# Optimization experiments

Measured on AMD Instinct MI355X. Metric: run time of the kernel, lower is better.

## Reference

```python
import jax, jax.numpy as jnp
import numpy as np

B, NQ, NKV = 2, 2048, 2048
QUERY_DIM = 1024
CONTEXT_DIM = 1024
HEADS = 16
DIM_HEAD = 64
INNER = HEADS * DIM_HEAD
SCALE = DIM_HEAD ** -0.5


def setup_inputs() -> dict:
    key = jax.random.key(0)
    ks = jax.random.split(key, 9)
    x = jax.random.normal(ks[0], (B, NQ, QUERY_DIM), dtype=jnp.float32)
    context = jax.random.normal(ks[1], (B, NKV, CONTEXT_DIM), dtype=jnp.float32)
    tgt_mask = jax.random.randint(ks[2], (B, 1, NQ, NKV), 0, 2, dtype=jnp.int32)
    src_mask = jax.random.randint(ks[3], (B, 1, NKV), 0, 2) > 0  # bool [b,1,j]
    w = 0.02
    Wq = jax.random.normal(ks[4], (INNER, QUERY_DIM), dtype=jnp.float32) * w
    Wk = jax.random.normal(ks[5], (INNER, CONTEXT_DIM), dtype=jnp.float32) * w
    Wv = jax.random.normal(ks[6], (INNER, CONTEXT_DIM), dtype=jnp.float32) * w
    Wo = jax.random.normal(ks[7], (QUERY_DIM, INNER), dtype=jnp.float32) * w
    bo = jax.random.normal(ks[8], (QUERY_DIM,), dtype=jnp.float32) * w
    return {"x": x, "context": context, "tgt_mask": tgt_mask, "src_mask": src_mask,
            "Wq": Wq, "Wk": Wk, "Wv": Wv, "Wo": Wo, "bo": bo}


def reference(x, context, tgt_mask, src_mask, Wq, Wk, Wv, Wo, bo):
    b, nq, _ = x.shape
    nkv = context.shape[1]
    # Linear projections (torch Linear: y = x @ W.T), split into heads: b n (h d) -> b h n d
    q = jnp.einsum('bnc,ec->bne', x, Wq).reshape(b, nq, HEADS, DIM_HEAD).transpose(0, 2, 1, 3)
    k = jnp.einsum('bmc,ec->bme', context, Wk).reshape(b, nkv, HEADS, DIM_HEAD).transpose(0, 2, 1, 3)
    v = jnp.einsum('bmc,ec->bme', context, Wv).reshape(b, nkv, HEADS, DIM_HEAD).transpose(0, 2, 1, 3)
    sim = jnp.einsum('bhid,bhjd->bhij', q, k) * SCALE
    neg = -jnp.finfo(sim.dtype).max
    sim = jnp.where(tgt_mask == 0, neg, sim)                 # tgt_mask [b,1,i,j]
    sim = jnp.where(src_mask[:, None, :], sim, neg)          # src_mask [b,1,j] -> [b,1,1,j]
    attn = jax.nn.softmax(sim, axis=-1)
    out = jnp.einsum('bhij,bhjd->bhid', attn, v)
    out = out.transpose(0, 2, 1, 3).reshape(b, nq, INNER)    # b h n d -> b n (h d)
    return jnp.einsum('bne,oe->bno', out, Wo) + bo           # dropout=0 at inference
```

## Files before the change

kernel.cpp:

```cpp
#include <hip/hip_runtime.h>

typedef short short8 __attribute__((ext_vector_type(8)));
typedef float f32x4 __attribute__((ext_vector_type(4)));
typedef float f32x16 __attribute__((ext_vector_type(16)));
typedef unsigned u32x4 __attribute__((ext_vector_type(4)));

#define GLOAD_LDS(src, dst) \
  __builtin_amdgcn_global_load_lds((const __attribute__((address_space(1))) void*)(src), \
                                   (__attribute__((address_space(3))) void*)(dst), 16, 0, 0)

__device__ __forceinline__ unsigned short f2b(float f){
  __bf16 h = (__bf16)f;
  return __builtin_bit_cast(unsigned short, h);
}
__device__ __forceinline__ unsigned pk2(float a, float b){
  unsigned r;
  asm("v_cvt_pk_bf16_f32 %0, %1, %2" : "=v"(r) : "v"(a), "v"(b));
  return r;
}
__device__ __forceinline__ float fexp2(float x){
  return __builtin_amdgcn_exp2f(x);
}
__device__ __forceinline__ float b2f(unsigned short u){
  union { unsigned u; float f; } cv;
  cv.u = ((unsigned)u) << 16;
  return cv.f;
}

__global__ void detect_mask_dtype(const int* __restrict__ src, int* __restrict__ flag){
  const int t = threadIdx.x;
  unsigned f = 0;
  #pragma unroll
  for (int i = 0; i < 16; i++)
    f |= (((const unsigned*)src)[t * 16 + i] > 1u) ? 1u : 0u;
  const unsigned long long any = __ballot(f != 0u);
  if (t == 0) *flag = any ? 1 : 0;
}

__global__ __launch_bounds__(256) void prep(const float* __restrict__ x, const float* __restrict__ ctx,
    const float* __restrict__ wq, const float* __restrict__ wk, const float* __restrict__ wv,
    const float* __restrict__ wo, const int* __restrict__ tgt, const void* __restrict__ srcm,
    const int* __restrict__ flag,
    unsigned short* __restrict__ xb, unsigned short* __restrict__ cb, unsigned short* __restrict__ wqb,
    unsigned short* __restrict__ wkvb, unsigned short* __restrict__ wob,
    unsigned long long* __restrict__ mp){
  const int blk = blockIdx.x;
  if (blk < 12288){
    const int i = blk * 256 + threadIdx.x;
    const float* src; unsigned short* dst; int so, doff;
    if (i < 1048576)      { src = x;   dst = xb;   so = i;           doff = so; }
    else if (i < 2097152) { src = ctx; dst = cb;   so = i - 1048576; doff = so; }
    else if (i < 2359296) { src = wq;  dst = wqb;  so = i - 2097152; doff = so; }
    else if (i < 2621440) { src = wk;  dst = wkvb; so = i - 2359296; doff = so; }
    else if (i < 2883584) { src = wv;  dst = wkvb; so = i - 2621440; doff = so + 262144; }
    else                  { src = wo;  dst = wob;  so = i - 2883584; doff = so; }
    const float4 v = reinterpret_cast<const float4*>(src)[so];
    ushort4 o;
    o.x = f2b(v.x); o.y = f2b(v.y); o.z = f2b(v.z); o.w = f2b(v.w);
    reinterpret_cast<ushort4*>(dst)[doff] = o;
  } else {
    size_t gt = (size_t)(blk - 12288) * 256 + threadIdx.x;
    int j = (int)(gt & 2047);
    size_t bi = gt >> 11;
    int b = (int)(bi >> 11);
    bool s;
    if (*flag) s = ((const unsigned char*)srcm)[b * 2048 + j] != 0;
    else       s = ((const int*)srcm)[b * 2048 + j] != 0;
    bool bit = (tgt[gt] != 0) && s;
    unsigned long long m = __ballot(bit ? 1 : 0);
    if ((threadIdx.x & 63) == 0) mp[gt >> 6] = m;
  }
}

__global__ __launch_bounds__(256) void masktr(const unsigned long long* __restrict__ mp,
                                              unsigned* __restrict__ mpT2){
  const int tile = blockIdx.x * 4 + (threadIdx.x >> 6);
  const int lane = threadIdx.x & 63;
  const int b  = tile >> 10;
  const int it = (tile >> 5) & 31;
  const int jt = tile & 31;
  unsigned long long xv = mp[((size_t)b * 2048 + it * 64 + lane) * 32 + jt];
  const unsigned long long A0 = 0x00000000FFFFFFFFull, A1 = 0x0000FFFF0000FFFFull,
                           A2 = 0x00FF00FF00FF00FFull, A3 = 0x0F0F0F0F0F0F0F0Full,
                           A4 = 0x3333333333333333ull, A5 = 0x5555555555555555ull;
#define TRSTEP(K, A) { \
    unsigned long long y = __shfl_xor(xv, K); \
    xv = (lane & (K)) ? (((y >> (K)) & (A)) | (xv & ~(A))) \
                      : ((xv & (A)) | ((y & (A)) << (K))); }
  TRSTEP(32, A0) TRSTEP(16, A1) TRSTEP(8, A2) TRSTEP(4, A3) TRSTEP(2, A4) TRSTEP(1, A5)
#undef TRSTEP
  unsigned* dst = mpT2 + (((size_t)b * 32 + jt) * 64 + it * 2) * 64 + lane;
  dst[0]  = (unsigned)xv;
  dst[64] = (unsigned)(xv >> 32);
}

#define G_DECLS \
  const int tid = threadIdx.x; \
  const int lane = tid & 63, wid = tid >> 6; \
  const int l15 = lane & 15, l4 = lane >> 4; \
  const int wm = wid >> 1, wn = wid & 1; \
  __shared__ unsigned short lA[3][128 * 32]; \
  __shared__ unsigned short lB[3][128 * 32]; \
  f32x4 acc[4][4] = {}; \
  const int r0 = tid >> 2, q0 = tid & 3; \
  const int r1 = (tid + 256) >> 2; \
  const unsigned short* a0p = A  + (size_t)(m0 + r0) * 1024 + q0 * 8; \
  const unsigned short* a1p = A  + (size_t)(m0 + r1) * 1024 + q0 * 8; \
  const unsigned short* b0p = Bw + (size_t)(n0 + r0) * 1024 + q0 * 8; \
  const unsigned short* b1p = Bw + (size_t)(n0 + r1) * 1024 + q0 * 8; \
  const int d0 = (wid * 64) * 8, d1 = (wid * 64 + 256) * 8;

#define G_STAGE(K0, BUF) { \
    GLOAD_LDS(a0p + (K0), &lA[BUF][d0]); \
    GLOAD_LDS(a1p + (K0), &lA[BUF][d1]); \
    GLOAD_LDS(b0p + (K0), &lB[BUF][d0]); \
    GLOAD_LDS(b1p + (K0), &lB[BUF][d1]); }

#define GCOMPUTE(BR) { \
  short8 af[4], bf[4]; \
  _Pragma("unroll") for (int m = 0; m < 4; m++) \
    af[m] = *reinterpret_cast<const short8*>(&lA[BR][(wm * 64 + m * 16 + l15) * 32 + l4 * 8]); \
  _Pragma("unroll") for (int n = 0; n < 4; n++) \
    bf[n] = *reinterpret_cast<const short8*>(&lB[BR][(wn * 64 + n * 16 + l15) * 32 + l4 * 8]); \
  _Pragma("unroll") for (int m = 0; m < 4; m++) \
    _Pragma("unroll") for (int n = 0; n < 4; n++) \
      acc[m][n] = __builtin_amdgcn_mfma_f32_16x16x32_bf16(af[m], bf[n], acc[m][n], 0, 0, 0); \
}

#define GITER(T, BR, BS, VM) { \
  asm volatile("s_waitcnt vmcnt(" #VM ")\n\ts_barrier" ::: "memory"); \
  if ((T) < 30) G_STAGE(((T) + 2) * 32, BS) \
  GCOMPUTE(BR) \
}

#define G_LOOP \
  G_STAGE(0, 0) \
  G_STAGE(32, 1) \
  for (int u = 0; u < 30; u += 3){ \
    GITER(u, 0, 2, 4) \
    GITER(u + 1, 1, 0, 4) \
    GITER(u + 2, 2, 1, 4) \
  } \
  GITER(30, 0, 2, 4) \
  GITER(31, 1, 0, 0)

__global__ __launch_bounds__(256, 3) void gemm_qkv(const unsigned short* __restrict__ xb,
                                                const unsigned short* __restrict__ cbuf,
                                                const unsigned short* __restrict__ wqb,
                                                const unsigned short* __restrict__ wkvb,
                                                unsigned short* __restrict__ qws,
                                                unsigned short* __restrict__ kws,
                                                unsigned short* __restrict__ vtw){
  const int f = blockIdx.x;
  const unsigned short *A, *Bw;
  int m0, n0, mode;
  if (f < 256){ A = xb;   Bw = wqb;  m0 = (f >> 3) * 128;  n0 = (f & 7) * 128;  mode = 0; }
  else { const int g = f - 256;
         A = cbuf; Bw = wkvb; m0 = (g >> 4) * 128;  n0 = (g & 15) * 128; mode = 1; }
  G_DECLS
  G_LOOP

  const int eb = n0 + wn * 64;
  const int mb = m0 + wm * 64 + l4 * 4;
  #pragma unroll
  for (int n = 0; n < 4; n++){
    const int e = eb + n * 16 + l15;
    #pragma unroll
    for (int m = 0; m < 4; m++){
      const int mm = mb + m * 16;
      if (mode == 0){
        const int h = e >> 6, d = e & 63;
        #pragma unroll
        for (int r = 0; r < 4; r++){
          const int row = mm + r, b = row >> 11, nn = row & 2047;
          qws[(((size_t)b * 16 + h) * 2048 + nn) * 64 + d] = f2b(acc[m][n][r] * 0.18033688011112042f);
        }
      } else {
        if (e < 1024){
          const int h = e >> 6, d = e & 63;
          #pragma unroll
          for (int r = 0; r < 4; r++){
            const int row = mm + r, b = row >> 11, nn = row & 2047;
            kws[(((size_t)b * 16 + h) * 2048 + nn) * 64 + d] = f2b(acc[m][n][r]);
          }
        } else {
          const int ee = e - 1024, h = ee >> 6, d = ee & 63;
          const int b = mm >> 11, nn = mm & 2047;
          ushort4 pk;
          pk.x = f2b(acc[m][n][0]); pk.y = f2b(acc[m][n][1]);
          pk.z = f2b(acc[m][n][2]); pk.w = f2b(acc[m][n][3]);
          *reinterpret_cast<ushort4*>(&vtw[(((size_t)b * 16 + h) * 64 + d) * 2048 + nn]) = pk;
        }
      }
    }
  }
}

__global__ __launch_bounds__(256, 3) void gemm_o(const unsigned short* __restrict__ A,
                                              const unsigned short* __restrict__ Bw,
                                              float* __restrict__ fout,
                                              const float* __restrict__ bias){
  const int m0 = blockIdx.y * 128, n0 = blockIdx.x * 128;
  G_DECLS
  G_LOOP

  const int eb = n0 + wn * 64;
  const int mb = m0 + wm * 64 + l4 * 4;
  #pragma unroll
  for (int n = 0; n < 4; n++){
    const int e = eb + n * 16 + l15;
    const float bv = bias[e];
    #pragma unroll
    for (int m = 0; m < 4; m++){
      const int mm = mb + m * 16;
      #pragma unroll
      for (int r = 0; r < 4; r++)
        fout[(size_t)(mm + r) * 1024 + e] = acc[m][n][r] + bv;
    }
  }
}

#define A_STAGE(T, BUF) { \
    const int jj = jbase + (T) * 64; \
    GLOAD_LDS(kb + (size_t)(jj + sr0) * 64 + sc0 * 8, &lK[BUF][dk0]); \
    GLOAD_LDS(kb + (size_t)(jj + sr1) * 64 + sc1 * 8, &lK[BUF][dk1]); \
    GLOAD_LDS(vb + (size_t)sr0 * 2048 + jj + sc0 * 8, &lV[BUF][dk0]); \
    GLOAD_LDS(vb + (size_t)sr1 * 2048 + jj + sc1 * 8, &lV[BUF][dk1]); }

#define A_COMPUTE(BR, T) { \
  const char* kbase = (const char*)lK[BR]; \
  f32x16 st0 = {}, st1 = {}; \
  __builtin_amdgcn_s_setprio(1); \
  _Pragma("unroll") for (int ks = 0; ks < 4; ks++){ \
    const short8 a0 = *reinterpret_cast<const short8*>(kbase + (((l31) * 128 + ks * 32 + hi * 16) ^ sw)); \
    st0 = __builtin_amdgcn_mfma_f32_32x32x16_bf16(a0, qf[ks], st0, 0, 0, 0); \
  } \
  _Pragma("unroll") for (int ks = 0; ks < 4; ks++){ \
    const short8 a1 = *reinterpret_cast<const short8*>(kbase + (((l31 + 32) * 128 + ks * 32 + hi * 16) ^ sw)); \
    st1 = __builtin_amdgcn_mfma_f32_32x32x16_bf16(a1, qf[ks], st1, 0, 0, 0); \
  } \
  __builtin_amdgcn_s_setprio(0); \
  const unsigned* mt = mt0 + (size_t)(T) * 4096; \
  _Pragma("unroll") for (int r = 0; r < 16; r++){ \
    const int dj = (r & 3) + 8 * (r >> 2); \
    const unsigned long long mk0 = (unsigned long long)mt[dj] | ((unsigned long long)mt[dj + 4] << 32); \
    const unsigned long long mk1 = (unsigned long long)mt[dj + 32] | ((unsigned long long)mt[dj + 36] << 32); \
    float v0, v1; \
    asm("v_cndmask_b32 %0, %1, %2, %3" : "=v"(v0) : "v"(negv), "v"((float)st0[r]), "s"(mk0)); \
    asm("v_cndmask_b32 %0, %1, %2, %3" : "=v"(v1) : "v"(negv), "v"((float)st1[r]), "s"(mk1)); \
    st0[r] = fexp2(v0); \
    st1[r] = fexp2(v1); \
  } \
  float s8[8]; \
  _Pragma("unroll") for (int i = 0; i < 8; i++) \
    s8[i] = (st0[i] + st0[i + 8]) + (st1[i] + st1[i + 8]); \
  float psum = ((s8[0] + s8[1]) + (s8[2] + s8[3])) + ((s8[4] + s8[5]) + (s8[6] + s8[7])); \
  psum += __shfl_xor(psum, 32); \
  l_i += psum; \
  const char* vbase = (const char*)lV[BR]; \
  _Pragma("unroll") for (int ks = 0; ks < 4; ks++){ \
    unsigned A0, B0, A1, B1; \
    if (ks < 2){ \
      A0 = pk2(st0[8 * ks + 0], st0[8 * ks + 1]); \
      B0 = pk2(st0[8 * ks + 2], st0[8 * ks + 3]); \
      A1 = pk2(st0[8 * ks + 4], st0[8 * ks + 5]); \
      B1 = pk2(st0[8 * ks + 6], st0[8 * ks + 7]); \
    } else { \
      A0 = pk2(st1[8 * (ks - 2) + 0], st1[8 * (ks - 2) + 1]); \
      B0 = pk2(st1[8 * (ks - 2) + 2], st1[8 * (ks - 2) + 3]); \
      A1 = pk2(st1[8 * (ks - 2) + 4], st1[8 * (ks - 2) + 5]); \
      B1 = pk2(st1[8 * (ks - 2) + 6], st1[8 * (ks - 2) + 7]); \
    } \
    asm("v_permlane32_swap_b32 %0, %1" : "+v"(A0), "+v"(A1)); \
    asm("v_permlane32_swap_b32 %0, %1" : "+v"(B0), "+v"(B1)); \
    const short8 pf = __builtin_bit_cast(short8, (u32x4){A0, B0, A1, B1}); \
    __builtin_amdgcn_s_setprio(1); \
    const short8 va0 = *reinterpret_cast<const short8*>(vbase + (((l31) * 128 + ks * 32 + hi * 16) ^ sw)); \
    o0_ = __builtin_amdgcn_mfma_f32_32x32x16_bf16(va0, pf, o0_, 0, 0, 0); \
    const short8 va1 = *reinterpret_cast<const short8*>(vbase + (((l31 + 32) * 128 + ks * 32 + hi * 16) ^ sw)); \
    o1_ = __builtin_amdgcn_mfma_f32_32x32x16_bf16(va1, pf, o1_, 0, 0, 0); \
    __builtin_amdgcn_s_setprio(0); \
  } \
}

__global__ __launch_bounds__(256, 4) void attn(const unsigned short* __restrict__ qw,
                                            const unsigned short* __restrict__ kw,
                                            const unsigned short* __restrict__ vtw,
                                            const unsigned* __restrict__ mpT2,
                                            unsigned short* __restrict__ opb,
                                            float* __restrict__ lsum){
  const int f = blockIdx.x;
  const int xcd = f & 7, slot = f >> 3;
  const int bh = xcd * 4 + (slot & 3);
  const int r2 = slot >> 2;
  const int qtile = r2 >> 1, kvh = r2 & 1;
  const int b = bh >> 4;
  const int qbase = qtile * 128;
  const int jbase = kvh * 1024;
  const int tid = threadIdx.x, wid = tid >> 6, lane = tid & 63;
  const int l31 = lane & 31, hi = lane >> 5;
  __shared__ unsigned short lK[2][64 * 64];
  __shared__ unsigned short lV[2][64 * 64];

  const int qrow = qbase + wid * 32 + l31;
  const unsigned short* qp = qw + ((size_t)bh * 2048 + qrow) * 64 + hi * 8;
  short8 qf[4];
  #pragma unroll
  for (int ks = 0; ks < 4; ks++)
    qf[ks] = *reinterpret_cast<const short8*>(qp + ks * 16);

  const int sr0 = tid >> 3,          sc0 = (tid & 7) ^ (sr0 & 7);
  const int sr1 = (tid + 256) >> 3,  sc1 = ((tid + 256) & 7) ^ (sr1 & 7);
  const unsigned short* kb = kw  + (size_t)bh * 2048 * 64;
  const unsigned short* vb = vtw + (size_t)bh * 64 * 2048;
  const int dk0 = (wid * 64) * 8, dk1 = (wid * 64 + 256) * 8;

  const int widu = __builtin_amdgcn_readfirstlane(wid);
  const int qw32 = qtile * 4 + widu;
  const unsigned* mt0 = mpT2 + (((size_t)b * 32 + kvh * 16) * 64 + qw32) * 64;

  float l_i = 0.f;
  f32x16 o0_ = {}, o1_ = {};
  const int sw = (l31 & 7) << 4;
  const float negv = -3.0e38f;

  A_STAGE(0, 0)
  __syncthreads();

  int cb_ = 0;
  for (int t = 0; t < 16; t++){
    if (t < 15) A_STAGE(t + 1, cb_ ^ 1)
    A_COMPUTE(cb_, t)
    if (t < 15) __syncthreads();
    cb_ ^= 1;
  }

  const int row = wid * 32 + l31;
  const int pidx = (bh * 16 + qtile) * 2 + kvh;
  unsigned short* opr = opb + (size_t)pidx * 8192 + row * 64;
  #pragma unroll
  for (int rq = 0; rq < 4; rq++){
    uint2 w0, w1;
    w0.x = pk2(o0_[rq * 4 + 0], o0_[rq * 4 + 1]); w0.y = pk2(o0_[rq * 4 + 2], o0_[rq * 4 + 3]);
    w1.x = pk2(o1_[rq * 4 + 0], o1_[rq * 4 + 1]); w1.y = pk2(o1_[rq * 4 + 2], o1_[rq * 4 + 3]);
    *reinterpret_cast<uint2*>(opr + rq * 8 + hi * 4)      = w0;
    *reinterpret_cast<uint2*>(opr + 32 + rq * 8 + hi * 4) = w1;
  }
  if (!hi)
    lsum[pidx * 128 + row] = l_i;
}

__global__ __launch_bounds__(256) void combine(const unsigned short* __restrict__ opb,
                                               const float* __restrict__ lsum,
                                               unsigned short* __restrict__ ao){
  const int g = blockIdx.x;
  const int bh = g >> 4, qtile = g & 15;
  const int b = bh >> 4, h = bh & 15;
  const int row = threadIdx.x >> 1;
  const int dh = (threadIdx.x & 1) * 32;
  const float l = lsum[(g * 2 + 0) * 128 + row] + lsum[(g * 2 + 1) * 128 + row];
  const float inv = 1.f / l;
  const unsigned short* p0 = opb + ((size_t)(g * 2 + 0)) * 8192 + row * 64 + dh;
  const unsigned short* p1 = opb + ((size_t)(g * 2 + 1)) * 8192 + row * 64 + dh;
  unsigned short* o = ao + ((size_t)b * 2048 + qtile * 128 + row) * 1024 + h * 64 + dh;
  #pragma unroll
  for (int i = 0; i < 4; i++){
    short8 v0 = *reinterpret_cast<const short8*>(p0 + i * 8);
    short8 v1 = *reinterpret_cast<const short8*>(p1 + i * 8);
    ushort4 wa, wb;
    wa.x = f2b((b2f((unsigned short)v0[0]) + b2f((unsigned short)v1[0])) * inv);
    wa.y = f2b((b2f((unsigned short)v0[1]) + b2f((unsigned short)v1[1])) * inv);
    wa.z = f2b((b2f((unsigned short)v0[2]) + b2f((unsigned short)v1[2])) * inv);
    wa.w = f2b((b2f((unsigned short)v0[3]) + b2f((unsigned short)v1[3])) * inv);
    wb.x = f2b((b2f((unsigned short)v0[4]) + b2f((unsigned short)v1[4])) * inv);
    wb.y = f2b((b2f((unsigned short)v0[5]) + b2f((unsigned short)v1[5])) * inv);
    wb.z = f2b((b2f((unsigned short)v0[6]) + b2f((unsigned short)v1[6])) * inv);
    wb.w = f2b((b2f((unsigned short)v0[7]) + b2f((unsigned short)v1[7])) * inv);
    reinterpret_cast<ushort4*>(o)[i * 2]     = wa;
    reinterpret_cast<ushort4*>(o)[i * 2 + 1] = wb;
  }
}

extern "C" void kernel_launch(void* const* d_in, const int* in_sizes, int n_in,
                              void* d_out, int out_size, void* d_ws, size_t ws_size,
                              hipStream_t stream){
  const float* x   = (const float*)d_in[0];
  const float* ctx = (const float*)d_in[1];
  const int*   tgt = (const int*)d_in[2];
  const void*  src = d_in[3];
  const float* Wq  = (const float*)d_in[4];
  const float* Wk  = (const float*)d_in[5];
  const float* Wv  = (const float*)d_in[6];
  const float* Wo  = (const float*)d_in[7];
  const float* bo  = (const float*)d_in[8];
  float* out = (float*)d_out;

  char* w = (char*)d_ws;
  unsigned short* xb   = (unsigned short*)(w);
  unsigned short* cb   = (unsigned short*)(w + (8u << 20));
  unsigned short* wqb  = (unsigned short*)(w + (16u << 20));
  unsigned short* wkvb = (unsigned short*)(w + (18u << 20));
  unsigned short* wob  = (unsigned short*)(w + (22u << 20));
  unsigned short* qws  = (unsigned short*)(w + (24u << 20));
  unsigned short* kws  = (unsigned short*)(w + (32u << 20));
  unsigned short* vtw  = (unsigned short*)(w + (40u << 20));
  unsigned long long* mp = (unsigned long long*)(w + (48u << 20));
  int* flag = (int*)(w + (49u << 20));
  unsigned short* opb  = (unsigned short*)(w + (50u << 20));
  unsigned* mpT2 = (unsigned*)(w + (16u << 20));
  float* lsum = (float*)(w + (8u << 20));
  unsigned short* ao = (unsigned short*)(w);

  detect_mask_dtype<<<1, 64, 0, stream>>>((const int*)src, flag);
  prep<<<12288 + 32768, 256, 0, stream>>>(x, ctx, Wq, Wk, Wv, Wo, tgt, src, flag,
                                          xb, cb, wqb, wkvb, wob, mp);
  gemm_qkv<<<768, 256, 0, stream>>>(xb, cb, wqb, wkvb, qws, kws, vtw);
  masktr<<<512, 256, 0, stream>>>(mp, mpT2);
  attn<<<1024, 256, 0, stream>>>(qws, kws, vtw, mpT2, opb, lsum);
  combine<<<512, 256, 0, stream>>>(opb, lsum, ao);
  gemm_o<<<dim3(8, 32), 256, 0, stream>>>(ao, wob, out, bo);
}
```

Baseline: 151.5 us.

## Split attention KV into four chunks with triple-buffered pipeline and inline mask detection

Attention now splits the KV range into four 512-wide chunks instead of two, doubling the grid to 2048 blocks, and combine merges four partial outputs. The K/V staging becomes a three-buffer ring with vmcnt-based waits that prefetch two tiles ahead, and launch bounds drop to 3 waves per SIMD. The per-tile cross-lane shuffle of the row sum moves to the end of the kernel. The separate mask-dtype detection kernel is removed, and each wave of prep now detects the mask dtype itself with a ballot. The aim is more parallelism and better load/compute overlap, at the cost of extra partial-output traffic and lower occupancy.

```diff
diff --git a/kernel.cpp b/kernel.cpp
--- a/kernel.cpp
+++ b/kernel.cpp
@@ -27,20 +27,9 @@
   return cv.f;
 }
 
-__global__ void detect_mask_dtype(const int* __restrict__ src, int* __restrict__ flag){
-  const int t = threadIdx.x;
-  unsigned f = 0;
-  #pragma unroll
-  for (int i = 0; i < 16; i++)
-    f |= (((const unsigned*)src)[t * 16 + i] > 1u) ? 1u : 0u;
-  const unsigned long long any = __ballot(f != 0u);
-  if (t == 0) *flag = any ? 1 : 0;
-}
-
 __global__ __launch_bounds__(256) void prep(const float* __restrict__ x, const float* __restrict__ ctx,
     const float* __restrict__ wq, const float* __restrict__ wk, const float* __restrict__ wv,
     const float* __restrict__ wo, const int* __restrict__ tgt, const void* __restrict__ srcm,
-    const int* __restrict__ flag,
     unsigned short* __restrict__ xb, unsigned short* __restrict__ cb, unsigned short* __restrict__ wqb,
     unsigned short* __restrict__ wkvb, unsigned short* __restrict__ wob,
     unsigned long long* __restrict__ mp){
@@ -63,9 +52,12 @@
     int j = (int)(gt & 2047);
     size_t bi = gt >> 11;
     int b = (int)(bi >> 11);
+    const int j0 = j & ~255;
+    const unsigned wv32 = ((const unsigned*)srcm)[((b * 2048 + j0) >> 2) + (threadIdx.x & 63)];
+    const bool u8mode = __ballot(wv32 > 1u) != 0ull;
     bool s;
-    if (*flag) s = ((const unsigned char*)srcm)[b * 2048 + j] != 0;
-    else       s = ((const int*)srcm)[b * 2048 + j] != 0;
+    if (u8mode) s = ((const unsigned char*)srcm)[b * 2048 + j] != 0;
+    else        s = ((const int*)srcm)[b * 2048 + j] != 0;
     bool bit = (tgt[gt] != 0) && s;
     unsigned long long m = __ballot(bit ? 1 : 0);
     if ((threadIdx.x & 63) == 0) mp[gt >> 6] = m;
@@ -254,9 +246,7 @@
   float s8[8]; \
   _Pragma("unroll") for (int i = 0; i < 8; i++) \
     s8[i] = (st0[i] + st0[i + 8]) + (st1[i] + st1[i + 8]); \
-  float psum = ((s8[0] + s8[1]) + (s8[2] + s8[3])) + ((s8[4] + s8[5]) + (s8[6] + s8[7])); \
-  psum += __shfl_xor(psum, 32); \
-  l_i += psum; \
+  l_i += ((s8[0] + s8[1]) + (s8[2] + s8[3])) + ((s8[4] + s8[5]) + (s8[6] + s8[7])); \
   const char* vbase = (const char*)lV[BR]; \
   _Pragma("unroll") for (int ks = 0; ks < 4; ks++){ \
     unsigned A0, B0, A1, B1; \
@@ -283,7 +273,13 @@
   } \
 }
 
-__global__ __launch_bounds__(256, 4) void attn(const unsigned short* __restrict__ qw,
+#define A_ITER(T, BR, BS, VM) { \
+  asm volatile("s_waitcnt vmcnt(" #VM ")\n\ts_barrier" ::: "memory"); \
+  if ((T) < 6) A_STAGE((T) + 2, BS) \
+  A_COMPUTE(BR, T) \
+}
+
+__global__ __launch_bounds__(256, 3) void attn(const unsigned short* __restrict__ qw,
                                             const unsigned short* __restrict__ kw,
                                             const unsigned short* __restrict__ vtw,
                                             const unsigned* __restrict__ mpT2,
@@ -293,14 +289,14 @@
   const int xcd = f & 7, slot = f >> 3;
   const int bh = xcd * 4 + (slot & 3);
   const int r2 = slot >> 2;
-  const int qtile = r2 >> 1, kvh = r2 & 1;
+  const int qtile = r2 >> 2, kvh = r2 & 3;
   const int b = bh >> 4;
   const int qbase = qtile * 128;
-  const int jbase = kvh * 1024;
+  const int jbase = kvh * 512;
   const int tid = threadIdx.x, wid = tid >> 6, lane = tid & 63;
   const int l31 = lane & 31, hi = lane >> 5;
-  __shared__ unsigned short lK[2][64 * 64];
-  __shared__ unsigned short lV[2][64 * 64];
+  __shared__ unsigned short lK[3][64 * 64];
+  __shared__ unsigned short lV[3][64 * 64];
 
   const int qrow = qbase + wid * 32 + l31;
   const unsigned short* qp = qw + ((size_t)bh * 2048 + qrow) * 64 + hi * 8;
@@ -317,7 +313,7 @@
 
   const int widu = __builtin_amdgcn_readfirstlane(wid);
   const int qw32 = qtile * 4 + widu;
-  const unsigned* mt0 = mpT2 + (((size_t)b * 32 + kvh * 16) * 64 + qw32) * 64;
+  const unsigned* mt0 = mpT2 + (((size_t)b * 32 + kvh * 8) * 64 + qw32) * 64;
 
   float l_i = 0.f;
   f32x16 o0_ = {}, o1_ = {};
@@ -325,18 +321,19 @@
   const float negv = -3.0e38f;
 
   A_STAGE(0, 0)
-  __syncthreads();
-
-  int cb_ = 0;
-  for (int t = 0; t < 16; t++){
-    if (t < 15) A_STAGE(t + 1, cb_ ^ 1)
-    A_COMPUTE(cb_, t)
-    if (t < 15) __syncthreads();
-    cb_ ^= 1;
-  }
-
+  A_STAGE(1, 1)
+
+  for (int u = 0; u < 6; u += 3){
+    A_ITER(u,     0, 2, 4)
+    A_ITER(u + 1, 1, 0, 4)
+    A_ITER(u + 2, 2, 1, 4)
+  }
+  A_ITER(6, 0, 2, 4)
+  A_ITER(7, 1, 0, 0)
+
+  l_i += __shfl_xor(l_i, 32);
   const int row = wid * 32 + l31;
-  const int pidx = (bh * 16 + qtile) * 2 + kvh;
+  const int pidx = (bh * 16 + qtile) * 4 + kvh;
   unsigned short* opr = opb + (size_t)pidx * 8192 + row * 64;
   #pragma unroll
   for (int rq = 0; rq < 4; rq++){
@@ -358,24 +355,30 @@
   const int b = bh >> 4, h = bh & 15;
   const int row = threadIdx.x >> 1;
   const int dh = (threadIdx.x & 1) * 32;
-  const float l = lsum[(g * 2 + 0) * 128 + row] + lsum[(g * 2 + 1) * 128 + row];
+  const float l = (lsum[(g * 4 + 0) * 128 + row] + lsum[(g * 4 + 1) * 128 + row])
+                + (lsum[(g * 4 + 2) * 128 + row] + lsum[(g * 4 + 3) * 128 + row]);
   const float inv = 1.f / l;
-  const unsigned short* p0 = opb + ((size_t)(g * 2 + 0)) * 8192 + row * 64 + dh;
-  const unsigned short* p1 = opb + ((size_t)(g * 2 + 1)) * 8192 + row * 64 + dh;
+  const unsigned short* p0 = opb + ((size_t)(g * 4 + 0)) * 8192 + row * 64 + dh;
+  const unsigned short* p1 = opb + ((size_t)(g * 4 + 1)) * 8192 + row * 64 + dh;
+  const unsigned short* p2 = opb + ((size_t)(g * 4 + 2)) * 8192 + row * 64 + dh;
+  const unsigned short* p3 = opb + ((size_t)(g * 4 + 3)) * 8192 + row * 64 + dh;
   unsigned short* o = ao + ((size_t)b * 2048 + qtile * 128 + row) * 1024 + h * 64 + dh;
   #pragma unroll
   for (int i = 0; i < 4; i++){
     short8 v0 = *reinterpret_cast<const short8*>(p0 + i * 8);
     short8 v1 = *reinterpret_cast<const short8*>(p1 + i * 8);
+    short8 v2 = *reinterpret_cast<const short8*>(p2 + i * 8);
+    short8 v3 = *reinterpret_cast<const short8*>(p3 + i * 8);
     ushort4 wa, wb;
-    wa.x = f2b((b2f((unsigned short)v0[0]) + b2f((unsigned short)v1[0])) * inv);
-    wa.y = f2b((b2f((unsigned short)v0[1]) + b2f((unsigned short)v1[1])) * inv);
-    wa.z = f2b((b2f((unsigned short)v0[2]) + b2f((unsigned short)v1[2])) * inv);
-    wa.w = f2b((b2f((unsigned short)v0[3]) + b2f((unsigned short)v1[3])) * inv);
-    wb.x = f2b((b2f((unsigned short)v0[4]) + b2f((unsigned short)v1[4])) * inv);
-    wb.y = f2b((b2f((unsigned short)v0[5]) + b2f((unsigned short)v1[5])) * inv);
-    wb.z = f2b((b2f((unsigned short)v0[6]) + b2f((unsigned short)v1[6])) * inv);
-    wb.w = f2b((b2f((unsigned short)v0[7]) + b2f((unsigned short)v1[7])) * inv);
+    #pragma unroll
+    for (int e = 0; e < 4; e++){
+      const float sa = (b2f((unsigned short)v0[e]) + b2f((unsigned short)v1[e]))
+                     + (b2f((unsigned short)v2[e]) + b2f((unsigned short)v3[e]));
+      ((unsigned short*)&wa)[e] = f2b(sa * inv);
+      const float sb = (b2f((unsigned short)v0[e + 4]) + b2f((unsigned short)v1[e + 4]))
+                     + (b2f((unsigned short)v2[e + 4]) + b2f((unsigned short)v3[e + 4]));
+      ((unsigned short*)&wb)[e] = f2b(sb * inv);
+    }
     reinterpret_cast<ushort4*>(o)[i * 2]     = wa;
     reinterpret_cast<ushort4*>(o)[i * 2 + 1] = wb;
   }
@@ -405,18 +408,16 @@
   unsigned short* kws  = (unsigned short*)(w + (32u << 20));
   unsigned short* vtw  = (unsigned short*)(w + (40u << 20));
   unsigned long long* mp = (unsigned long long*)(w + (48u << 20));
-  int* flag = (int*)(w + (49u << 20));
   unsigned short* opb  = (unsigned short*)(w + (50u << 20));
   unsigned* mpT2 = (unsigned*)(w + (16u << 20));
   float* lsum = (float*)(w + (8u << 20));
   unsigned short* ao = (unsigned short*)(w);
 
-  detect_mask_dtype<<<1, 64, 0, stream>>>((const int*)src, flag);
-  prep<<<12288 + 32768, 256, 0, stream>>>(x, ctx, Wq, Wk, Wv, Wo, tgt, src, flag,
+  prep<<<12288 + 32768, 256, 0, stream>>>(x, ctx, Wq, Wk, Wv, Wo, tgt, src,
                                           xb, cb, wqb, wkvb, wob, mp);
   gemm_qkv<<<768, 256, 0, stream>>>(xb, cb, wqb, wkvb, qws, kws, vtw);
   masktr<<<512, 256, 0, stream>>>(mp, mpT2);
-  attn<<<1024, 256, 0, stream>>>(qws, kws, vtw, mpT2, opb, lsum);
+  attn<<<2048, 256, 0, stream>>>(qws, kws, vtw, mpT2, opb, lsum);
   combine<<<512, 256, 0, stream>>>(opb, lsum, ao);
   gemm_o<<<dim3(8, 32), 256, 0, stream>>>(ao, wob, out, bo);
 }
```

After: 199.3 us. 1.32x slower.
